# Kernel tuning notes

Hardware: AMD Instinct MI355X
Metric: run time of the kernel (lower is better)

Reference implementation:

```python
import jax, jax.numpy as jnp
import numpy as np

B, T, E = 16, 1024, 1024
G, N, D = 4, 8, 128
V = 2048


def setup_inputs() -> dict:
    key = jax.random.key(0)
    k1, k2, k3, k4 = jax.random.split(key, 4)
    x_emb = jax.random.normal(k1, (B, T, E), dtype=jnp.float32)
    W_in = jax.random.normal(k2, (E, G * N * D), dtype=jnp.float32) / np.sqrt(E)
    R = jax.random.normal(k3, (G, N, D, D), dtype=jnp.float32) / np.sqrt(D)
    b = jnp.zeros((G, N, D), dtype=jnp.float32)
    W_proj = jax.random.normal(k4, (V, N * D), dtype=jnp.float32) / np.sqrt(D)
    b_proj = jnp.zeros((V,), dtype=jnp.float32)
    return {"x_emb": x_emb, "W_in": W_in, "R": R, "b": b, "W_proj": W_proj, "b_proj": b_proj}


def reference(x_emb, W_in, R, b, W_proj, b_proj):
    # Input projection for all timesteps at once: [B,T,G,N,D]
    Bx, Tx, Ex = x_emb.shape
    Wx = jnp.einsum('bte,eg->btg', x_emb, W_in).reshape(Bx, Tx, G, N, D)

    def step(carry, wx_t):
        h, c = carry  # [B,N,D] each
        # per-head matrix recurrence: R[g] @ h  -> [B,G,N,D]
        gates = wx_t + jnp.einsum('gnde,bne->bgnd', R, h) + b
        i = jax.nn.sigmoid(gates[:, 0])
        f = jax.nn.sigmoid(gates[:, 1])
        z = jnp.tanh(gates[:, 2])
        o = jax.nn.sigmoid(gates[:, 3])
        c_new = f * c + i * z
        h_new = o * jnp.tanh(c_new)
        return (h_new, c_new), h_new

    h0 = jnp.zeros((Bx, N, D), dtype=x_emb.dtype)
    c0 = jnp.zeros((Bx, N, D), dtype=x_emb.dtype)
    (hN, cN), hs = jax.lax.scan(step, (h0, c0), jnp.swapaxes(Wx, 0, 1))  # hs: [T,B,N,D]
    h_flat = jnp.swapaxes(hs, 0, 1).reshape(Bx, Tx, N * D)
    logits = jnp.einsum('btn,vn->btv', h_flat, W_proj) + b_proj
    return logits
```

## Files before the change

kernel.cpp:

```cpp
#include <hip/hip_runtime.h>
#include <hip/hip_bf16.h>

#define DEV __device__ __forceinline__

using bf16 = __hip_bfloat16;
typedef __attribute__((ext_vector_type(8))) short short8v;
typedef __attribute__((ext_vector_type(4))) float f32x4;

constexpr int Bq = 16, Tq = 1024, Eq = 1024, Gq = 4, Nq = 8, Dq = 128, Vq = 2048;
constexpr int M1 = Bq * Tq;
constexpr int N1q = Gq * Nq * Dq;
constexpr int K1 = Eq;
constexpr int K2 = Nq * Dq;
constexpr int N2 = Vq;

DEV unsigned short bfu(float x) {
  union { bf16 h; unsigned short u; } cv;
  cv.h = __float2bfloat16(x);
  return cv.u;
}

DEV float rcp_(float x) { return __builtin_amdgcn_rcpf(x); }
DEV float sigm(float x) { return rcp_(1.0f + __expf(-x)); }
DEV float tanh_(float x) { return fmaf(2.0f, rcp_(1.0f + __expf(-2.0f * x)), -1.0f); }

#define GLD16(gp, lp)                                                       \
  __builtin_amdgcn_global_load_lds(                                        \
      (const __attribute__((address_space(1))) void*)(gp),                 \
      (__attribute__((address_space(3))) void*)(lp), 16, 0, 0)

__global__ __launch_bounds__(256) void cast_f32_bf16(const float* __restrict__ s,
                                                     bf16* __restrict__ d, int n4) {
  const int i = blockIdx.x * 256 + threadIdx.x;
  if (i >= n4) return;
  const float4 v = ((const float4*)s)[i];
  ushort4 u;
  u.x = bfu(v.x); u.y = bfu(v.y); u.z = bfu(v.z); u.w = bfu(v.w);
  ((ushort4*)d)[i] = u;
}

__global__ __launch_bounds__(256) void transpose_cast(const float* __restrict__ s,
                                                      bf16* __restrict__ d,
                                                      int SK, int SN) {
  __shared__ float t[32][33];
  const int n0 = blockIdx.x * 32, k0 = blockIdx.y * 32;
  const int tx = threadIdx.x & 31, ty = threadIdx.x >> 5;
#pragma unroll
  for (int i = 0; i < 32; i += 8)
    t[ty + i][tx] = s[(size_t)(k0 + ty + i) * SN + n0 + tx];
  __syncthreads();
#pragma unroll
  for (int i = 0; i < 32; i += 8)
    d[(size_t)(n0 + ty + i) * SK + k0 + tx] = __float2bfloat16(t[tx][ty + i]);
}

template <int MODE>
__global__ __launch_bounds__(256) void gemm_bt(const bf16* __restrict__ A,
                                               const bf16* __restrict__ Bt,
                                               void* __restrict__ Cout,
                                               const float* __restrict__ bp,
                                               int K, int N) {
  __shared__ bf16 As[128 * 32];
  __shared__ bf16 Bs[128 * 32];
  const int m0 = blockIdx.y * 128, n0 = blockIdx.x * 128;
  const int tid = threadIdx.x;
  const int lane = tid & 63, w = tid >> 6;
  const int wm = w >> 1, wn = w & 1;

  const int srow = lane >> 2, scol = (lane & 3) * 8;
  const int ca = w * 2;
  const bf16* Ag0 = A + (size_t)(m0 + ca * 16 + srow) * K + scol;
  const bf16* Ag1 = Ag0 + (size_t)16 * K;
  const bf16* Bg0 = Bt + (size_t)(n0 + ca * 16 + srow) * K + scol;
  const bf16* Bg1 = Bg0 + (size_t)16 * K;
  bf16* Al0 = As + ca * 512;
  bf16* Al1 = Al0 + 512;
  bf16* Bl0 = Bs + ca * 512;
  bf16* Bl1 = Bl0 + 512;

  f32x4 acc[4][4] = {};

  const int rr = lane & 15;
  const int kb = (lane >> 4) * 8;

  for (int k0 = 0; k0 < K; k0 += 32) {
    GLD16(Ag0 + k0, Al0);
    GLD16(Ag1 + k0, Al1);
    GLD16(Bg0 + k0, Bl0);
    GLD16(Bg1 + k0, Bl1);
    __syncthreads();
    short8v af[4], bfr[4];
#pragma unroll
    for (int i = 0; i < 4; ++i) {
      af[i]  = *(const short8v*)&As[(wm * 64 + i * 16 + rr) * 32 + kb];
      bfr[i] = *(const short8v*)&Bs[(wn * 64 + i * 16 + rr) * 32 + kb];
    }
#pragma unroll
    for (int i = 0; i < 4; ++i)
#pragma unroll
      for (int j = 0; j < 4; ++j)
        acc[i][j] = __builtin_amdgcn_mfma_f32_16x16x32_bf16(af[i], bfr[j], acc[i][j], 0, 0, 0);
    __syncthreads();
  }

  const int crow = (lane >> 4) * 4, ccol = lane & 15;
  if constexpr (MODE == 2) {
    bf16* C = (bf16*)Cout;
#pragma unroll
    for (int i = 0; i < 4; ++i)
#pragma unroll
      for (int j = 0; j < 4; ++j) {
        const int col = n0 + wn * 64 + j * 16 + ccol;
        const int g = col >> 10, nn = (col >> 7) & 7, dd = col & 127;
#pragma unroll
        for (int jj = 0; jj < 4; ++jj) {
          const int row = m0 + wm * 64 + i * 16 + crow + jj;
          const int b = row >> 10, t = row & 1023;
          C[(((size_t)(b * 8 + nn) * 1024 + t) << 9) + dd * 4 + g] =
              __float2bfloat16(acc[i][j][jj]);
        }
      }
  } else {
    float* C = (float*)Cout;
    float bv[4];
#pragma unroll
    for (int j = 0; j < 4; ++j) bv[j] = bp[n0 + wn * 64 + j * 16 + ccol];
#pragma unroll
    for (int i = 0; i < 4; ++i)
#pragma unroll
      for (int j = 0; j < 4; ++j) {
        const size_t base =
            (size_t)(m0 + wm * 64 + i * 16 + crow) * N + (n0 + wn * 64 + j * 16 + ccol);
#pragma unroll
        for (int jj = 0; jj < 4; ++jj)
          C[base + (size_t)jj * N] = acc[i][j][jj] + bv[j];
      }
  }
}

__global__ __launch_bounds__(512) void lstm_mfma(const bf16* __restrict__ Wx,
                                                 const float* __restrict__ R,
                                                 const float* __restrict__ bias,
                                                 bf16* __restrict__ h_all) {
  const int wg = blockIdx.x;
  const int bb = wg >> 3;
  const int n = wg & 7;
  const int tid = threadIdx.x;
  const int w = tid >> 6, lane = tid & 63;
  const int lg = lane >> 4;
  const int lc = lane & 15;
  const int d = w * 16 + lc;

  short8v Bf[4][4];
#pragma unroll
  for (int g = 0; g < 4; ++g)
#pragma unroll
    for (int kf = 0; kf < 4; ++kf) {
      const float* rp = R + (size_t)((g * Nq + n) * Dq + d) * Dq + 32 * kf + 8 * lg;
      const float4 r0 = *(const float4*)rp;
      const float4 r1 = *(const float4*)(rp + 4);
      short8v bv;
      bv[0] = (short)bfu(r0.x); bv[1] = (short)bfu(r0.y);
      bv[2] = (short)bfu(r0.z); bv[3] = (short)bfu(r0.w);
      bv[4] = (short)bfu(r1.x); bv[5] = (short)bfu(r1.y);
      bv[6] = (short)bfu(r1.z); bv[7] = (short)bfu(r1.w);
      Bf[g][kf] = bv;
    }

  float bvf[4];
#pragma unroll
  for (int g = 0; g < 4; ++g) bvf[g] = bias[(g * Nq + n) * Dq + d];

  __shared__ __align__(16) bf16 hbuf[2][128];
  if (tid < 128) hbuf[0][tid] = __float2bfloat16(0.f);
  __syncthreads();

  const bf16* wx0 = Wx + ((size_t)(bb * 8 + n) << 19) + d * 4;
  bf16* hallp = h_all + ((size_t)(bb * Tq) * Nq + n) * Dq + d;

  ushort4 wxr[4];
#pragma unroll
  for (int u = 0; u < 4; ++u)
    wxr[u] = *(const ushort4*)(wx0 + ((size_t)u << 9));

  float c = 0.f;

  for (int t0 = 0; t0 < Tq; t0 += 4) {
#pragma unroll
    for (int u = 0; u < 4; ++u) {
      const int t = t0 + u;
      const bf16* hb = hbuf[t & 1];
      short8v Af[4];
#pragma unroll
      for (int kf = 0; kf < 4; ++kf)
        Af[kf] = *(const short8v*)(hb + 32 * kf + 8 * lg);

      float wxf[4];
      wxf[0] = __uint_as_float((unsigned)wxr[u].x << 16);
      wxf[1] = __uint_as_float((unsigned)wxr[u].y << 16);
      wxf[2] = __uint_as_float((unsigned)wxr[u].z << 16);
      wxf[3] = __uint_as_float((unsigned)wxr[u].w << 16);

      f32x4 a0[4], a1[4], a2[4], a3[4];
#pragma unroll
      for (int g = 0; g < 4; ++g) {
        const float pre = wxf[g] + bvf[g];
        a0[g][0] = pre; a0[g][1] = pre; a0[g][2] = pre; a0[g][3] = pre;
        a1[g] = {}; a2[g] = {}; a3[g] = {};
      }
#pragma unroll
      for (int g = 0; g < 4; ++g) {
        a0[g] = __builtin_amdgcn_mfma_f32_16x16x32_bf16(Af[0], Bf[g][0], a0[g], 0, 0, 0);
        a1[g] = __builtin_amdgcn_mfma_f32_16x16x32_bf16(Af[1], Bf[g][1], a1[g], 0, 0, 0);
        a2[g] = __builtin_amdgcn_mfma_f32_16x16x32_bf16(Af[2], Bf[g][2], a2[g], 0, 0, 0);
        a3[g] = __builtin_amdgcn_mfma_f32_16x16x32_bf16(Af[3], Bf[g][3], a3[g], 0, 0, 0);
      }

      {
        const int tp = (t + 4 < Tq) ? (t + 4) : (Tq - 1);
        wxr[u] = *(const ushort4*)(wx0 + ((size_t)tp << 9));
      }

      const float i_ = sigm((a0[0][0] + a1[0][0]) + (a2[0][0] + a3[0][0]));
      const float f_ = sigm((a0[1][0] + a1[1][0]) + (a2[1][0] + a3[1][0]));
      const float z_ = tanh_((a0[2][0] + a1[2][0]) + (a2[2][0] + a3[2][0]));
      const float o_ = sigm((a0[3][0] + a1[3][0]) + (a2[3][0] + a3[3][0]));
      c = f_ * c + i_ * z_;
      const float h = o_ * tanh_(c);
      const bf16 h16 = __float2bfloat16(h);

      if (lg == 0) {
        hbuf[(t + 1) & 1][d] = h16;
        hallp[(size_t)t * (Nq * Dq)] = h16;
      }
      __builtin_amdgcn_sched_barrier(0);
      asm volatile("s_waitcnt lgkmcnt(0)" ::: "memory");
      __builtin_amdgcn_sched_barrier(0);
      __builtin_amdgcn_s_barrier();
      __builtin_amdgcn_sched_barrier(0);
    }
  }
}

extern "C" void kernel_launch(void* const* d_in, const int* in_sizes, int n_in,
                              void* d_out, int out_size, void* d_ws, size_t ws_size,
                              hipStream_t stream) {
  const float* x_emb = (const float*)d_in[0];
  const float* W_in  = (const float*)d_in[1];
  const float* R     = (const float*)d_in[2];
  const float* bias  = (const float*)d_in[3];
  const float* W_prj = (const float*)d_in[4];
  const float* b_prj = (const float*)d_in[5];

  char* ws = (char*)d_ws;
  bf16* xb  = (bf16*)ws;
  bf16* WiT = (bf16*)(ws + (size_t)M1 * K1 * 2);
  bf16* Wpb = WiT + (size_t)N1q * K1;
  bf16* H   = Wpb + (size_t)N2 * K2;
  bf16* Wx = (bf16*)d_out;

  cast_f32_bf16<<<(M1 * K1 / 4 + 255) / 256, 256, 0, stream>>>(x_emb, xb, M1 * K1 / 4);
  transpose_cast<<<dim3(N1q / 32, K1 / 32), 256, 0, stream>>>(W_in, WiT, K1, N1q);
  cast_f32_bf16<<<(N2 * K2 / 4 + 255) / 256, 256, 0, stream>>>(W_prj, Wpb, N2 * K2 / 4);

  gemm_bt<2><<<dim3(N1q / 128, M1 / 128), 256, 0, stream>>>(
      xb, WiT, (void*)Wx, nullptr, K1, N1q);

  lstm_mfma<<<dim3(Bq * Nq), 512, 0, stream>>>(Wx, R, bias, H);

  gemm_bt<0><<<dim3(N2 / 128, M1 / 128), 256, 0, stream>>>(
      H, Wpb, d_out, b_prj, K2, N2);
}
```

Before: 829.7 us.

## Process two batch rows per LSTM block to interleave independent MFMA chains

Each recurrence workgroup now handles two batch elements (bb and bb+8) that share the same R fragments, so the grid shrinks from 128 to 64 blocks. The two independent MFMA and gate chains are interleaved so that each can fill the other's latency on the serial per-step critical path. The four per-k accumulators are also merged into a single chained accumulator for each gate. The trade-offs are fewer workgroups on the GPU, a serial dependency inside each gate's MFMA chain, and more register pressure.

```diff
diff --git a/kernel.cpp b/kernel.cpp
--- a/kernel.cpp
+++ b/kernel.cpp
@@ -171,67 +171,93 @@
 #pragma unroll
   for (int g = 0; g < 4; ++g) bvf[g] = bias[(g * Nq + n) * Dq + d];
 
-  __shared__ __align__(16) bf16 hbuf[2][128];
-  if (tid < 128) hbuf[0][tid] = __float2bfloat16(0.f);
+  __shared__ __align__(16) bf16 hbuf[2][2][128];
+  if (tid < 128) {
+    hbuf[0][0][tid] = __float2bfloat16(0.f);
+    hbuf[1][0][tid] = __float2bfloat16(0.f);
+  }
   __syncthreads();
 
-  const bf16* wx0 = Wx + ((size_t)(bb * 8 + n) << 19) + d * 4;
-  bf16* hallp = h_all + ((size_t)(bb * Tq) * Nq + n) * Dq + d;
-
-  ushort4 wxr[4];
-#pragma unroll
-  for (int u = 0; u < 4; ++u)
-    wxr[u] = *(const ushort4*)(wx0 + ((size_t)u << 9));
-
-  float c = 0.f;
+  const bf16* wxA = Wx + ((size_t)(bb * 8 + n) << 19) + d * 4;
+  const bf16* wxB = Wx + ((size_t)((bb + 8) * 8 + n) << 19) + d * 4;
+  bf16* hpA = h_all + ((size_t)(bb * Tq) * Nq + n) * Dq + d;
+  bf16* hpB = h_all + ((size_t)((bb + 8) * Tq) * Nq + n) * Dq + d;
+
+  ushort4 wxrA[4], wxrB[4];
+#pragma unroll
+  for (int u = 0; u < 4; ++u) {
+    wxrA[u] = *(const ushort4*)(wxA + ((size_t)u << 9));
+    wxrB[u] = *(const ushort4*)(wxB + ((size_t)u << 9));
+  }
+
+  float cA = 0.f, cB = 0.f;
 
   for (int t0 = 0; t0 < Tq; t0 += 4) {
 #pragma unroll
     for (int u = 0; u < 4; ++u) {
       const int t = t0 + u;
-      const bf16* hb = hbuf[t & 1];
-      short8v Af[4];
+      const bf16* hA = hbuf[0][t & 1];
+      const bf16* hB = hbuf[1][t & 1];
+      short8v AfA[4], AfB[4];
+#pragma unroll
+      for (int kf = 0; kf < 4; ++kf) {
+        AfA[kf] = *(const short8v*)(hA + 32 * kf + 8 * lg);
+        AfB[kf] = *(const short8v*)(hB + 32 * kf + 8 * lg);
+      }
+
+      float wxfA[4], wxfB[4];
+      wxfA[0] = __uint_as_float((unsigned)wxrA[u].x << 16);
+      wxfA[1] = __uint_as_float((unsigned)wxrA[u].y << 16);
+      wxfA[2] = __uint_as_float((unsigned)wxrA[u].z << 16);
+      wxfA[3] = __uint_as_float((unsigned)wxrA[u].w << 16);
+      wxfB[0] = __uint_as_float((unsigned)wxrB[u].x << 16);
+      wxfB[1] = __uint_as_float((unsigned)wxrB[u].y << 16);
+      wxfB[2] = __uint_as_float((unsigned)wxrB[u].z << 16);
+      wxfB[3] = __uint_as_float((unsigned)wxrB[u].w << 16);
+
+      f32x4 aA[4], aB[4];
+#pragma unroll
+      for (int g = 0; g < 4; ++g) {
+        const float pA = wxfA[g] + bvf[g];
+        const float pB = wxfB[g] + bvf[g];
+        aA[g][0] = pA; aA[g][1] = pA; aA[g][2] = pA; aA[g][3] = pA;
+        aB[g][0] = pB; aB[g][1] = pB; aB[g][2] = pB; aB[g][3] = pB;
+      }
 #pragma unroll
       for (int kf = 0; kf < 4; ++kf)
-        Af[kf] = *(const short8v*)(hb + 32 * kf + 8 * lg);
-
-      float wxf[4];
-      wxf[0] = __uint_as_float((unsigned)wxr[u].x << 16);
-      wxf[1] = __uint_as_float((unsigned)wxr[u].y << 16);
-      wxf[2] = __uint_as_float((unsigned)wxr[u].z << 16);
-      wxf[3] = __uint_as_float((unsigned)wxr[u].w << 16);
-
-      f32x4 a0[4], a1[4], a2[4], a3[4];
-#pragma unroll
-      for (int g = 0; g < 4; ++g) {
-        const float pre = wxf[g] + bvf[g];
-        a0[g][0] = pre; a0[g][1] = pre; a0[g][2] = pre; a0[g][3] = pre;
-        a1[g] = {}; a2[g] = {}; a3[g] = {};
-      }
-#pragma unroll
-      for (int g = 0; g < 4; ++g) {
-        a0[g] = __builtin_amdgcn_mfma_f32_16x16x32_bf16(Af[0], Bf[g][0], a0[g], 0, 0, 0);
-        a1[g] = __builtin_amdgcn_mfma_f32_16x16x32_bf16(Af[1], Bf[g][1], a1[g], 0, 0, 0);
-        a2[g] = __builtin_amdgcn_mfma_f32_16x16x32_bf16(Af[2], Bf[g][2], a2[g], 0, 0, 0);
-        a3[g] = __builtin_amdgcn_mfma_f32_16x16x32_bf16(Af[3], Bf[g][3], a3[g], 0, 0, 0);
-      }
+#pragma unroll
+        for (int g = 0; g < 4; ++g) {
+          aA[g] = __builtin_amdgcn_mfma_f32_16x16x32_bf16(AfA[kf], Bf[g][kf], aA[g], 0, 0, 0);
+          aB[g] = __builtin_amdgcn_mfma_f32_16x16x32_bf16(AfB[kf], Bf[g][kf], aB[g], 0, 0, 0);
+        }
 
       {
         const int tp = (t + 4 < Tq) ? (t + 4) : (Tq - 1);
-        wxr[u] = *(const ushort4*)(wx0 + ((size_t)tp << 9));
-      }
-
-      const float i_ = sigm((a0[0][0] + a1[0][0]) + (a2[0][0] + a3[0][0]));
-      const float f_ = sigm((a0[1][0] + a1[1][0]) + (a2[1][0] + a3[1][0]));
-      const float z_ = tanh_((a0[2][0] + a1[2][0]) + (a2[2][0] + a3[2][0]));
-      const float o_ = sigm((a0[3][0] + a1[3][0]) + (a2[3][0] + a3[3][0]));
-      c = f_ * c + i_ * z_;
-      const float h = o_ * tanh_(c);
-      const bf16 h16 = __float2bfloat16(h);
+        wxrA[u] = *(const ushort4*)(wxA + ((size_t)tp << 9));
+        wxrB[u] = *(const ushort4*)(wxB + ((size_t)tp << 9));
+      }
+
+      const float iA = sigm(aA[0][0]);
+      const float fA = sigm(aA[1][0]);
+      const float zA = tanh_(aA[2][0]);
+      const float oA = sigm(aA[3][0]);
+      cA = fA * cA + iA * zA;
+      const float hAv = oA * tanh_(cA);
+      const bf16 hA16 = __float2bfloat16(hAv);
+
+      const float iB = sigm(aB[0][0]);
+      const float fB = sigm(aB[1][0]);
+      const float zB = tanh_(aB[2][0]);
+      const float oB = sigm(aB[3][0]);
+      cB = fB * cB + iB * zB;
+      const float hBv = oB * tanh_(cB);
+      const bf16 hB16 = __float2bfloat16(hBv);
 
       if (lg == 0) {
-        hbuf[(t + 1) & 1][d] = h16;
-        hallp[(size_t)t * (Nq * Dq)] = h16;
+        hbuf[0][(t + 1) & 1][d] = hA16;
+        hbuf[1][(t + 1) & 1][d] = hB16;
+        hpA[(size_t)t * (Nq * Dq)] = hA16;
+        hpB[(size_t)t * (Nq * Dq)] = hB16;
       }
       __builtin_amdgcn_sched_barrier(0);
       asm volatile("s_waitcnt lgkmcnt(0)" ::: "memory");
@@ -266,7 +292,7 @@
   gemm_bt<2><<<dim3(N1q / 128, M1 / 128), 256, 0, stream>>>(
       xb, WiT, (void*)Wx, nullptr, K1, N1q);
 
-  lstm_mfma<<<dim3(Bq * Nq), 512, 0, stream>>>(Wx, R, bias, H);
+  lstm_mfma<<<dim3(64), 512, 0, stream>>>(Wx, R, bias, H);
 
   gemm_bt<0><<<dim3(N2 / 128, M1 / 128), 256, 0, stream>>>(
       H, Wpb, d_out, b_prj, K2, N2);
```

Result: slower. 1.181 ms (+42.3%).

## Batch all 16 sequences per head into one LSTM workgroup using full MFMA rows

Applied to the files above, without the earlier changes.

The recurrence kernel now runs one workgroup per head (8 total) instead of one per (batch, head) (128). All 16 batch rows fill the M dimension of each 16x16x32 MFMA, so every accumulator lane carries a useful value, where before only one row per tile was meaningful. The Wx layout from the first GEMM is reordered to [n,t,g,d,b] so each lane can fetch its four batch values directly. The gate bias is folded into that GEMM's epilogue, and the four K-slice accumulators are merged into a single chained accumulator. The trade-off is that only 8 CUs are active and each time step has a longer serial MFMA dependency chain.

```diff
diff --git a/kernel.cpp b/kernel.cpp
--- a/kernel.cpp
+++ b/kernel.cpp
@@ -112,12 +112,14 @@
       for (int j = 0; j < 4; ++j) {
         const int col = n0 + wn * 64 + j * 16 + ccol;
         const int g = col >> 10, nn = (col >> 7) & 7, dd = col & 127;
+        const float bvj = bp[(g * 8 + nn) * 128 + dd];
 #pragma unroll
         for (int jj = 0; jj < 4; ++jj) {
           const int row = m0 + wm * 64 + i * 16 + crow + jj;
           const int b = row >> 10, t = row & 1023;
-          C[(((size_t)(b * 8 + nn) * 1024 + t) << 9) + dd * 4 + g] =
-              __float2bfloat16(acc[i][j][jj]);
+          const size_t idx =
+              ((((size_t)nn * 1024 + t) * 4 + g) * 128 + dd) * 16 + b;
+          C[idx] = __float2bfloat16(acc[i][j][jj] + bvj);
         }
       }
   } else {
@@ -138,13 +140,10 @@
   }
 }
 
-__global__ __launch_bounds__(512) void lstm_mfma(const bf16* __restrict__ Wx,
-                                                 const float* __restrict__ R,
-                                                 const float* __restrict__ bias,
-                                                 bf16* __restrict__ h_all) {
-  const int wg = blockIdx.x;
-  const int bb = wg >> 3;
-  const int n = wg & 7;
+__global__ __launch_bounds__(512, 2) void lstm_mfma(const bf16* __restrict__ Wx,
+                                                    const float* __restrict__ R,
+                                                    bf16* __restrict__ h_all) {
+  const int n = blockIdx.x;
   const int tid = threadIdx.x;
   const int w = tid >> 6, lane = tid & 63;
   const int lg = lane >> 4;
@@ -167,72 +166,67 @@
       Bf[g][kf] = bv;
     }
 
-  float bvf[4];
-#pragma unroll
-  for (int g = 0; g < 4; ++g) bvf[g] = bias[(g * Nq + n) * Dq + d];
-
-  __shared__ __align__(16) bf16 hbuf[2][128];
-  if (tid < 128) hbuf[0][tid] = __float2bfloat16(0.f);
+  __shared__ __align__(16) unsigned short hl[2][16][136];
+  for (int i = tid; i < 16 * 136; i += 512) (&hl[0][0][0])[i] = 0;
   __syncthreads();
 
-  const bf16* wx0 = Wx + ((size_t)(bb * 8 + n) << 19) + d * 4;
-  bf16* hallp = h_all + ((size_t)(bb * Tq) * Nq + n) * Dq + d;
-
-  ushort4 wxr[4];
+  const bf16* wxb = Wx + ((size_t)n << 23) + d * 16 + lg * 4;
+  bf16* hout = h_all + n * 128 + d;
+
+  ushort4 wxr[4][4];
 #pragma unroll
   for (int u = 0; u < 4; ++u)
-    wxr[u] = *(const ushort4*)(wx0 + ((size_t)u << 9));
-
-  float c = 0.f;
+#pragma unroll
+    for (int g = 0; g < 4; ++g)
+      wxr[u][g] = *(const ushort4*)(wxb + ((size_t)u << 13) + (g << 11));
+
+  float cst[4] = {0.f, 0.f, 0.f, 0.f};
 
   for (int t0 = 0; t0 < Tq; t0 += 4) {
 #pragma unroll
     for (int u = 0; u < 4; ++u) {
       const int t = t0 + u;
-      const bf16* hb = hbuf[t & 1];
+      const unsigned short* hb = &hl[t & 1][0][0];
       short8v Af[4];
 #pragma unroll
       for (int kf = 0; kf < 4; ++kf)
-        Af[kf] = *(const short8v*)(hb + 32 * kf + 8 * lg);
-
-      float wxf[4];
-      wxf[0] = __uint_as_float((unsigned)wxr[u].x << 16);
-      wxf[1] = __uint_as_float((unsigned)wxr[u].y << 16);
-      wxf[2] = __uint_as_float((unsigned)wxr[u].z << 16);
-      wxf[3] = __uint_as_float((unsigned)wxr[u].w << 16);
-
-      f32x4 a0[4], a1[4], a2[4], a3[4];
+        Af[kf] = *(const short8v*)(hb + lc * 136 + kf * 32 + lg * 8);
+
+      f32x4 acc[4];
 #pragma unroll
       for (int g = 0; g < 4; ++g) {
-        const float pre = wxf[g] + bvf[g];
-        a0[g][0] = pre; a0[g][1] = pre; a0[g][2] = pre; a0[g][3] = pre;
-        a1[g] = {}; a2[g] = {}; a3[g] = {};
-      }
-#pragma unroll
-      for (int g = 0; g < 4; ++g) {
-        a0[g] = __builtin_amdgcn_mfma_f32_16x16x32_bf16(Af[0], Bf[g][0], a0[g], 0, 0, 0);
-        a1[g] = __builtin_amdgcn_mfma_f32_16x16x32_bf16(Af[1], Bf[g][1], a1[g], 0, 0, 0);
-        a2[g] = __builtin_amdgcn_mfma_f32_16x16x32_bf16(Af[2], Bf[g][2], a2[g], 0, 0, 0);
-        a3[g] = __builtin_amdgcn_mfma_f32_16x16x32_bf16(Af[3], Bf[g][3], a3[g], 0, 0, 0);
-      }
+        acc[g][0] = __uint_as_float((unsigned)wxr[u][g].x << 16);
+        acc[g][1] = __uint_as_float((unsigned)wxr[u][g].y << 16);
+        acc[g][2] = __uint_as_float((unsigned)wxr[u][g].z << 16);
+        acc[g][3] = __uint_as_float((unsigned)wxr[u][g].w << 16);
+      }
+#pragma unroll
+      for (int kf = 0; kf < 4; ++kf)
+#pragma unroll
+        for (int g = 0; g < 4; ++g)
+          acc[g] = __builtin_amdgcn_mfma_f32_16x16x32_bf16(Af[kf], Bf[g][kf], acc[g], 0, 0, 0);
 
       {
         const int tp = (t + 4 < Tq) ? (t + 4) : (Tq - 1);
-        wxr[u] = *(const ushort4*)(wx0 + ((size_t)tp << 9));
-      }
-
-      const float i_ = sigm((a0[0][0] + a1[0][0]) + (a2[0][0] + a3[0][0]));
-      const float f_ = sigm((a0[1][0] + a1[1][0]) + (a2[1][0] + a3[1][0]));
-      const float z_ = tanh_((a0[2][0] + a1[2][0]) + (a2[2][0] + a3[2][0]));
-      const float o_ = sigm((a0[3][0] + a1[3][0]) + (a2[3][0] + a3[3][0]));
-      c = f_ * c + i_ * z_;
-      const float h = o_ * tanh_(c);
-      const bf16 h16 = __float2bfloat16(h);
-
-      if (lg == 0) {
-        hbuf[(t + 1) & 1][d] = h16;
-        hallp[(size_t)t * (Nq * Dq)] = h16;
-      }
+#pragma unroll
+        for (int g = 0; g < 4; ++g)
+          wxr[u][g] = *(const ushort4*)(wxb + ((size_t)tp << 13) + (g << 11));
+      }
+
+#pragma unroll
+      for (int jj = 0; jj < 4; ++jj) {
+        const float i_ = sigm(acc[0][jj]);
+        const float f_ = sigm(acc[1][jj]);
+        const float z_ = tanh_(acc[2][jj]);
+        const float o_ = sigm(acc[3][jj]);
+        cst[jj] = f_ * cst[jj] + i_ * z_;
+        const float h = o_ * tanh_(cst[jj]);
+        const bf16 h16 = __float2bfloat16(h);
+        const int b = lg * 4 + jj;
+        hl[(t + 1) & 1][b][d] = ((unsigned short*)&h16)[0];
+        hout[((size_t)b << 20) + ((size_t)t << 10)] = h16;
+      }
+
       __builtin_amdgcn_sched_barrier(0);
       asm volatile("s_waitcnt lgkmcnt(0)" ::: "memory");
       __builtin_amdgcn_sched_barrier(0);
@@ -264,9 +258,9 @@
   cast_f32_bf16<<<(N2 * K2 / 4 + 255) / 256, 256, 0, stream>>>(W_prj, Wpb, N2 * K2 / 4);
 
   gemm_bt<2><<<dim3(N1q / 128, M1 / 128), 256, 0, stream>>>(
-      xb, WiT, (void*)Wx, nullptr, K1, N1q);
-
-  lstm_mfma<<<dim3(Bq * Nq), 512, 0, stream>>>(Wx, R, bias, H);
+      xb, WiT, (void*)Wx, bias, K1, N1q);
+
+  lstm_mfma<<<dim3(Nq), 512, 0, stream>>>(Wx, R, H);
 
   gemm_bt<0><<<dim3(N2 / 128, M1 / 128), 256, 0, stream>>>(
       H, Wpb, d_out, b_prj, K2, N2);
```

Measured after the change: 1.497 ms. 1.8x slower.
